# Performance work log

Hardware: AMD Instinct MI355X
Metric: run time of the kernel (lower is better)

## Reference

```python
import jax, jax.numpy as jnp
import numpy as np

BS, P, D, C, ND, K, NC, H = 32, 196, 512, 100, 51, 50, 800, 8
LAMBDA, BETA, EPS = 0.5, 5.5, 1e-5


def _ln(x, g, b):
    m = x.mean(-1, keepdims=True)
    v = jnp.mean((x - m) ** 2, axis=-1, keepdims=True)
    return (x - m) / jnp.sqrt(v + EPS) * g + b


def _norm(x):
    return x / jnp.linalg.norm(x, axis=-1, keepdims=True)


def _bonder(x, kv, Wq, Wk, Wv, Wo, ln1_g, ln1_b, ln2_g, ln2_b, W1, b1, W2, b2):
    # cross-attn block: queries = text prompts [B,N,d], kv = retrieved patch feats [B,M,d]
    B, N, d = x.shape
    M = kv.shape[1]
    dh = d // H
    q = (_ln(x, ln1_g, ln1_b) @ Wq).reshape(B, N, H, dh)
    k = (kv @ Wk).reshape(B, M, H, dh)
    v = (kv @ Wv).reshape(B, M, H, dh)
    att = jax.nn.softmax(jnp.einsum('bnhd,bmhd->bhnm', q, k) / np.sqrt(dh).astype(np.float32), axis=-1)
    o = jnp.einsum('bhnm,bmhd->bnhd', att, v).reshape(B, N, d) @ Wo
    x = x + o
    h = _ln(x, ln2_g, ln2_b)
    return x + jax.nn.gelu(h @ W1 + b1) @ W2 + b2


def _dense_logits(gfeat, local, all_text, mean_text, topk):
    # gfeat [b,d], local [b,p,d], all_text [C,n,d], mean_text [C,d]
    base = gfeat @ mean_text.T                                   # [b,C]
    w = jnp.einsum('bd,bpd->bp', gfeat, local)                   # [b,p]
    atf = jnp.transpose(all_text, (1, 0, 2))                     # [n,C,d]
    v = jax.nn.softmax(jnp.einsum('cd,ncd->nc', mean_text, atf), axis=0)  # [n,C]
    sim = jnp.einsum('bpd,ncd->bcpn', local, atf)                # [b,C,p,n]
    vals, idx = jax.lax.top_k(jnp.transpose(sim, (0, 1, 3, 2)), topk)     # over patch dim
    sim_topk = jnp.transpose(vals, (0, 1, 3, 2))                 # [b,C,k,n]
    idx = jnp.transpose(idx, (0, 1, 3, 2))                       # [b,C,k,n]
    idx_w = idx[:, 0, :, 0]                                      # [b,k]
    w_topk = jax.nn.softmax(jnp.take_along_axis(w, idx_w, axis=1), axis=-1)  # [b,k]
    weight = jnp.einsum('bk,nc->bckn', w_topk, v)                # [b,C,k,n]
    return base + jnp.sum(sim_topk * weight, axis=(-2, -1))


def setup_inputs() -> dict:
    key = jax.random.key(0)
    ks = jax.random.split(key, 12)
    s = 0.02
    labels = jax.random.randint(ks[10], (BS,), 0, C)
    cache_labels = jax.random.randint(ks[11], (NC,), 0, C)
    return {
        'local_feat': jax.random.normal(ks[0], (BS, P, D)),
        'Wa': jnp.eye(D) + s * jax.random.normal(ks[1], (D, D)),
        'text_cache': jax.random.normal(ks[2], (C, ND, D)),
        'Wq': s * jax.random.normal(ks[3], (D, D)),
        'Wk': s * jax.random.normal(ks[4], (D, D)),
        'Wv': s * jax.random.normal(ks[5], (D, D)),
        'Wo': s * jax.random.normal(ks[6], (D, D)),
        'ln1_g': jnp.ones((D,)), 'ln1_b': jnp.zeros((D,)),
        'ln2_g': jnp.ones((D,)), 'ln2_b': jnp.zeros((D,)),
        'W1': s * jax.random.normal(ks[7], (D, 4 * D)), 'b1': jnp.zeros((4 * D,)),
        'W2': s * jax.random.normal(ks[8], (4 * D, D)), 'b2': jnp.zeros((D,)),
        'logit_scale': jnp.asarray(np.log(1.0 / 0.07), jnp.float32),
        'ensemble_scale': jnp.asarray(-2.0, jnp.float32),
        'raw_cache_local_feats': jax.random.normal(ks[9], (NC, P, D)),
        'cache_values': jax.nn.one_hot(cache_labels, C, dtype=jnp.float32),
        'labels': labels,
        'cache_labels': cache_labels,
    }


def reference(local_feat, Wa, text_cache, Wq, Wk, Wv, Wo, ln1_g, ln1_b, ln2_g, ln2_b,
              W1, b1, W2, b2, logit_scale, ensemble_scale, raw_cache_local_feats,
              cache_values, labels, cache_labels):
    bs = local_feat.shape[0]
    adapted_local = _norm(local_feat @ Wa.T)                      # [b,p,d]
    adapted_global = _norm(adapted_local.mean(axis=1))            # [b,d]
    base_text_mean = _norm(jax.lax.stop_gradient(text_cache).mean(axis=1))  # [C,d]
    sim_to_text = jax.lax.stop_gradient(adapted_local @ base_text_mean.T)   # [b,p,C]
    sim_target = sim_to_text[jnp.arange(bs), :, labels]           # [b,p]
    topk_idx = jax.lax.top_k(sim_target, K)[1]
    botk_idx = jax.lax.top_k(-sim_target, K)[1]
    topk_feats = jnp.take_along_axis(adapted_local, topk_idx[:, :, None], axis=1)  # [b,K,d]
    botk_feats = jnp.take_along_axis(adapted_local, botk_idx[:, :, None], axis=1)
    # training branch: bonder on ground-truth class prompts, scatter into bias_full
    l2p = text_cache[labels]                                      # [b,ND,d]
    text_bias = _bonder(l2p, jax.lax.stop_gradient(topk_feats),
                        Wq, Wk, Wv, Wo, ln1_g, ln1_b, ln2_g, ln2_b, W1, b1, W2, b2)
    bias_full = jnp.zeros((bs, C, ND, D), local_feat.dtype).at[jnp.arange(bs), labels].set(text_bias)
    bias_avg = bias_full.mean(axis=0)                             # [C,ND,d]
    refined = text_cache + LAMBDA * bias_avg
    refined_norm = _norm(refined)
    refined_mean_norm = _norm(refined_norm.mean(axis=1))
    ls = jnp.exp(logit_scale)
    inter = ls * _dense_logits(adapted_global, adapted_local, refined_norm, refined_mean_norm, K)
    # tip-adapter cache branch
    cache_adapted = _norm(raw_cache_local_feats @ Wa.T)           # [Nc,p,d]
    cache_sim = jax.lax.stop_gradient(cache_adapted @ base_text_mean.T)
    cache_sim_target = cache_sim[jnp.arange(cache_sim.shape[0]), :, cache_labels]
    cache_topk_idx = jax.lax.top_k(cache_sim_target, K)[1]
    cache_topk_feats = jnp.take_along_axis(cache_adapted, cache_topk_idx[:, :, None], axis=1)
    cache_keys = _norm(cache_topk_feats.mean(axis=1))             # [Nc,d]
    query_keys = _norm(topk_feats.mean(axis=1))                   # [b,d]
    affinity = jnp.exp(-BETA * (1.0 - query_keys @ cache_keys.T))
    intra = affinity @ cache_values                               # [b,C]
    scale = jax.nn.sigmoid(ensemble_scale)
    logits = inter * (1 - scale) + intra * ls * scale
    return (logits, inter, intra, adapted_global, topk_feats, botk_feats, refined_norm)
```

## Files before the change

### kernel.cpp

```cpp
#include <hip/hip_runtime.h>
#include <math.h>

#define DEV static __device__ __forceinline__

typedef __attribute__((ext_vector_type(8))) short short8v;
typedef __attribute__((ext_vector_type(8))) _Float16 half8v;
typedef __attribute__((ext_vector_type(4))) float f32x4;

DEV unsigned encf(float f){ unsigned b=__float_as_uint(f); return b ^ (0x80000000u | (unsigned)((int)b>>31)); }
DEV unsigned long long pkvi(float v, int idx){
  return ((unsigned long long)encf(v)<<32) | (unsigned long long)(0xffffffffu - (unsigned)idx);
}
DEV unsigned long long wave_max_ull(unsigned long long u){
  #pragma unroll
  for (int m=1;m<64;m<<=1){ unsigned long long o = __shfl_xor(u, m); if (o>u) u=o; }
  return u;
}
DEV float wave_sum(float v){
  #pragma unroll
  for (int m=32;m;m>>=1) v += __shfl_xor(v, m);
  return v;
}
DEV float blk_sum256(float v, float* scr){
  v = wave_sum(v);
// ... 76 lines not shown
      for (int i=0;i<8;++i)
        #pragma unroll
        for (int j=0;j<8;++j) acc[i][j] = fmaf(a[i], bb[j], acc[i][j]);
    }
    __syncthreads();
  }

  #pragma unroll
  for (int i=0;i<8;++i){
    int gr = row0 + ((i<4)? (ty*4+i) : (64+ty*4+i-4));
    if (gr >= M) continue;
    #pragma unroll
    for (int jb=0;jb<2;++jb){
      int gc = col0 + (jb? (64+tx*4) : (tx*4));
      float4 vv;
      vv.x = acc[i][jb*4+0]; vv.y = acc[i][jb*4+1]; vv.z = acc[i][jb*4+2]; vv.w = acc[i][jb*4+3];
      if (EPI & 1){
        const float4 bv = *(const float4*)(bias + gc);
        vv.x += bv.x; vv.y += bv.y; vv.z += bv.z; vv.w += bv.w;
      }
      if (EPI & 2){
        vv.x = gelu_f(vv.x); vv.y = gelu_f(vv.y); vv.z = gelu_f(vv.z); vv.w = gelu_f(vv.w);
      }
      if (EPI & 4){
        const float4 rv = *(const float4*)(resid + (size_t)gr*N + gc);
        vv.x += rv.x; vv.y += rv.y; vv.z += rv.z; vv.w += rv.w;
      }
      *(float4*)(Cp + (size_t)gr*N + gc) = vv;
    }
  }
}

template<bool TRANS, bool SUBI>
__global__ __launch_bounds__(256) void k_convw(const float* __restrict__ W,
    unsigned short* __restrict__ hi, unsigned short* __restrict__ lo, int R, int C){
  int n = blockIdx.x;
  int K = TRANS ? R : C;
  for (int k = threadIdx.x; k < K; k += 256){
    float x = TRANS ? W[(size_t)k*C + n] : W[(size_t)n*C + k];
    if (SUBI && k==n) x -= 1.f;
    unsigned short h = f2bf(x);
    hi[(size_t)n*K + k] = h;
    if (lo) lo[(size_t)n*K + k] = f2bf(x - bf2f(h));
  }
}

__global__ __launch_bounds__(256) void k_convw4(
  const float* __restrict__ Wq, const float* __restrict__ Wk,
  const float* __restrict__ Wv, const float* __restrict__ Wo,
  unsigned short* __restrict__ qh, unsigned short* __restrict__ ql,
  unsigned short* __restrict__ kh, unsigned short* __restrict__ kl,
  unsigned short* __restrict__ vh, unsigned short* __restrict__ vl,
  unsigned short* __restrict__ oh, unsigned short* __restrict__ ol)
{
  int n = blockIdx.x;
  const float* W; unsigned short *hi, *lo;
  switch(blockIdx.y){
    case 0: W=Wq; hi=qh; lo=ql; break;
    case 1: W=Wk; hi=kh; lo=kl; break;
    case 2: W=Wv; hi=vh; lo=vl; break;
    default: W=Wo; hi=oh; lo=ol; break;
  }
  for (int k = threadIdx.x; k < 512; k += 256){
    float x = W[(size_t)k*512 + n];
    unsigned short h = f2bf(x);
    hi[(size_t)n*512 + k] = h;
    lo[(size_t)n*512 + k] = f2bf(x - bf2f(h));
  }
}

__global__ __launch_bounds__(256) void k_convd2(const float* __restrict__ Wa, unsigned short* __restrict__ Dfrag){
  int e = blockIdx.x;
  int tile = e>>4, lr = e&15;
  for (int d = threadIdx.x; d < 512; d += 256){
    float x = Wa[(size_t)e*512 + d] - (e==d ? 1.f : 0.f);
    union { _Float16 hh; unsigned short u; } cv;
    cv.hh = (_Float16)x;
    int ks = d>>5, q = (d>>3)&3, el = d&7;
    Dfrag[(size_t)(((tile*16+ks)*64 + q*16 + lr)*8 + el)] = cv.u;
  }
}

template<int EPI>
__global__ __launch_bounds__(256,2) void gemmMF(
  const float* __restrict__ A, const unsigned short* __restrict__ Bhi,
  const unsigned short* __restrict__ Blo, float* __restrict__ Cp,
  const int M, const int N, const int K,
  const float* __restrict__ bias, const float* __restrict__ resid)
{
  __shared__ __align__(16) char sm[32768];
  const int t = threadIdx.x, lane = t&63, wid = t>>6;
  const int row0 = blockIdx.x*128, col0 = blockIdx.y*128;
  f32x4 acc[2][8];
  #pragma unroll
  for (int i=0;i<2;++i)
    #pragma unroll
    for (int j=0;j<8;++j) acc[i][j] = (f32x4){0.f,0.f,0.f,0.f};

  int offA[2], offB[8];
  #pragma unroll
  for (int mt=0; mt<2; ++mt){
    int row = (2*wid+mt)*16 + (lane&15);
    int sp = (lane>>4) ^ ((row>>1)&3);
    offA[mt] = row*64 + sp*16;
  }
  #pragma unroll
  for (int nt=0; nt<8; ++nt){
    int row = nt*16 + (lane&15);
    int sp = (lane>>4) ^ ((row>>1)&3);
    offB[nt] = row*64 + sp*16;
  }

  const int nks = K >> 5;
  for (int ks=0; ks<nks; ++ks){
    #pragma unroll
    for (int i=0;i<2;++i){
      int s = i*256 + t, row = s>>2, sl2 = s&3, phys = sl2 ^ ((row>>1)&3);
      int gr = row0 + row;
      float4 p0 = make_float4(0.f,0.f,0.f,0.f), p1 = p0;
      if (gr < M){
        const float* gp = A + (size_t)gr*K + ks*32 + sl2*8;
        p0 = *(const float4*)gp; p1 = *(const float4*)(gp+4);
      }
      float xs[8] = {p0.x,p0.y,p0.z,p0.w,p1.x,p1.y,p1.z,p1.w};
      union { unsigned short u[8]; float4 f; } uh, ul;
      #pragma unroll
      for (int u=0;u<8;++u){
        unsigned short h = f2bf(xs[u]);
        uh.u[u] = h;
        ul.u[u] = f2bf(xs[u] - bf2f(h));
      }
      *(float4*)(sm + row*64 + phys*16) = uh.f;
      *(float4*)(sm + 8192 + row*64 + phys*16) = ul.f;
    }
    #pragma unroll
    for (int i=0;i<2;++i){
      int s = i*256 + t, row = s>>2, sl2 = s&3, slog = sl2 ^ ((row>>1)&3);
      size_t goff = (size_t)(col0+row)*K + ks*32 + slog*8;
      gld16(Bhi + goff, sm + 16384 + (i*256 + wid*64)*16);
      gld16(Blo + goff, sm + 24576 + (i*256 + wid*64)*16);
    }
    __syncthreads();
    short8v ah0 = *(short8v*)(sm + offA[0]);
    short8v ah1 = *(short8v*)(sm + offA[1]);
    short8v al0 = *(short8v*)(sm + 8192 + offA[0]);
    short8v al1 = *(short8v*)(sm + 8192 + offA[1]);
    #pragma unroll
    for (int nt=0; nt<8; ++nt){
      short8v bh = *(short8v*)(sm + 16384 + offB[nt]);
      short8v bl = *(short8v*)(sm + 24576 + offB[nt]);
      acc[0][nt] = __builtin_amdgcn_mfma_f32_16x16x32_bf16(ah0, bh, acc[0][nt], 0,0,0);
      acc[0][nt] = __builtin_amdgcn_mfma_f32_16x16x32_bf16(ah0, bl, acc[0][nt], 0,0,0);
      acc[0][nt] = __builtin_amdgcn_mfma_f32_16x16x32_bf16(al0, bh, acc[0][nt], 0,0,0);
      acc[1][nt] = __builtin_amdgcn_mfma_f32_16x16x32_bf16(ah1, bh, acc[1][nt], 0,0,0);
      acc[1][nt] = __builtin_amdgcn_mfma_f32_16x16x32_bf16(ah1, bl, acc[1][nt], 0,0,0);
      acc[1][nt] = __builtin_amdgcn_mfma_f32_16x16x32_bf16(al1, bh, acc[1][nt], 0,0,0);
    }
    __syncthreads();
  }

  #pragma unroll
  for (int mt=0; mt<2; ++mt){
    #pragma unroll
    for (int nt=0; nt<8; ++nt){
      int n = col0 + nt*16 + (lane&15);
      int mb = row0 + (2*wid+mt)*16 + (lane>>4)*4;
      #pragma unroll
      for (int j=0;j<4;++j){
        int m = mb + j;
        if (m < M){
          float v = acc[mt][nt][j];
          if (EPI & 1) v += bias[n];
          if (EPI & 2) v = gelu_f(v);
          if (EPI & 4) v += resid[(size_t)m*N + n];
          Cp[(size_t)m*N + n] = v;
        }
      }
    }
  }
}

__global__ __launch_bounds__(256,2) void gemmQKV(
  const float* __restrict__ ln1x, const float* __restrict__ otk,
  const unsigned short* __restrict__ qh, const unsigned short* __restrict__ ql,
  const unsigned short* __restrict__ kh, const unsigned short* __restrict__ kl,
  const unsigned short* __restrict__ vh, const unsigned short* __restrict__ vl,
  float* __restrict__ qb, float* __restrict__ kb, float* __restrict__ vbuf)
{
  __shared__ __align__(16) char sm[32768];
  const int z = blockIdx.z;
  const float* A = (z==0)? ln1x : otk;
  const unsigned short* Bhi = (z==0)? qh : (z==1? kh : vh);
  const unsigned short* Blo = (z==0)? ql : (z==1? kl : vl);
  float* Cp = (z==0)? qb : (z==1? kb : vbuf);
  const int M = (z==0)? 1632 : 1600;
  const int N = 512, K = 512;
  const int t = threadIdx.x, lane = t&63, wid = t>>6;
  const int row0 = blockIdx.x*128, col0 = blockIdx.y*128;
  f32x4 acc[2][8];
  #pragma unroll
  for (int i=0;i<2;++i)
    #pragma unroll
    for (int j=0;j<8;++j) acc[i][j] = (f32x4){0.f,0.f,0.f,0.f};

  int offA[2], offB[8];
  #pragma unroll
  for (int mt=0; mt<2; ++mt){
    int row = (2*wid+mt)*16 + (lane&15);
    int sp = (lane>>4) ^ ((row>>1)&3);
    offA[mt] = row*64 + sp*16;
  }
  #pragma unroll
  for (int nt=0; nt<8; ++nt){
    int row = nt*16 + (lane&15);
    int sp = (lane>>4) ^ ((row>>1)&3);
    offB[nt] = row*64 + sp*16;
  }

  for (int ks=0; ks<16; ++ks){
    #pragma unroll
    for (int i=0;i<2;++i){
      int s = i*256 + t, row = s>>2, sl2 = s&3, phys = sl2 ^ ((row>>1)&3);
      int gr = row0 + row;
      float4 p0 = make_float4(0.f,0.f,0.f,0.f), p1 = p0;
      if (gr < M){
        const float* gp = A + (size_t)gr*K + ks*32 + sl2*8;
        p0 = *(const float4*)gp; p1 = *(const float4*)(gp+4);
      }
      float xs[8] = {p0.x,p0.y,p0.z,p0.w,p1.x,p1.y,p1.z,p1.w};
      union { unsigned short u[8]; float4 f; } uh, ul;
      #pragma unroll
      for (int u=0;u<8;++u){
        unsigned short h = f2bf(xs[u]);
        uh.u[u] = h;
        ul.u[u] = f2bf(xs[u] - bf2f(h));
      }
      *(float4*)(sm + row*64 + phys*16) = uh.f;
      *(float4*)(sm + 8192 + row*64 + phys*16) = ul.f;
    }
    #pragma unroll
    for (int i=0;i<2;++i){
      int s = i*256 + t, row = s>>2, sl2 = s&3, slog = sl2 ^ ((row>>1)&3);
      size_t goff = (size_t)(col0+row)*K + ks*32 + slog*8;
      gld16(Bhi + goff, sm + 16384 + (i*256 + wid*64)*16);
      gld16(Blo + goff, sm + 24576 + (i*256 + wid*64)*16);
    }
    __syncthreads();
    short8v ah0 = *(short8v*)(sm + offA[0]);
    short8v ah1 = *(short8v*)(sm + offA[1]);
    short8v al0 = *(short8v*)(sm + 8192 + offA[0]);
    short8v al1 = *(short8v*)(sm + 8192 + offA[1]);
    #pragma unroll
    for (int nt=0; nt<8; ++nt){
      short8v bh = *(short8v*)(sm + 16384 + offB[nt]);
      short8v bl = *(short8v*)(sm + 24576 + offB[nt]);
      acc[0][nt] = __builtin_amdgcn_mfma_f32_16x16x32_bf16(ah0, bh, acc[0][nt], 0,0,0);
      acc[0][nt] = __builtin_amdgcn_mfma_f32_16x16x32_bf16(ah0, bl, acc[0][nt], 0,0,0);
      acc[0][nt] = __builtin_amdgcn_mfma_f32_16x16x32_bf16(al0, bh, acc[0][nt], 0,0,0);
      acc[1][nt] = __builtin_amdgcn_mfma_f32_16x16x32_bf16(ah1, bh, acc[1][nt], 0,0,0);
      acc[1][nt] = __builtin_amdgcn_mfma_f32_16x16x32_bf16(ah1, bl, acc[1][nt], 0,0,0);
      acc[1][nt] = __builtin_amdgcn_mfma_f32_16x16x32_bf16(al1, bh, acc[1][nt], 0,0,0);
    }
    __syncthreads();
  }

  #pragma unroll
  for (int mt=0; mt<2; ++mt){
    #pragma unroll
    for (int nt=0; nt<8; ++nt){
      int n = col0 + nt*16 + (lane&15);
      int mb = row0 + (2*wid+mt)*16 + (lane>>4)*4;
      #pragma unroll
      for (int j=0;j<4;++j){
        int m = mb + j;
        if (m < M) Cp[(size_t)m*N + n] = acc[mt][nt][j];
      }
    }
  }
}

__global__ __launch_bounds__(512,1) void k_un7(
  const float* __restrict__ raw, const unsigned short* __restrict__ Dfrag,
  const float* __restrict__ zm, const int* __restrict__ clab,
  float* __restrict__ cdot, float* __restrict__ norm2)
{
  __shared__ __align__(16) char Alds[131072];
  __shared__ float n2sq[128];
  __shared__ float n2x[4][128];
  const int t = threadIdx.x, lane = t&63;
  const int wid = t>>6, wm = wid>>2, wn = wid&3;
  const int m0 = blockIdx.x*128;

  {
    const int row = t>>2, sl = t&3;
    const int slg = sl ^ ((row>>1)&3);
    const float* rp = raw + ((size_t)(m0+row))*512 + slg*8;
    const float* zp = zm + (size_t)clab[(m0+row)/196]*512 + slg*8;
    float sq=0.f, cd=0.f;
    for (int ks=0; ks<16; ++ks){
      float4 p0 = *(const float4*)(rp + ks*32);
      float4 p1 = *(const float4*)(rp + ks*32 + 4);
      float4 z0 = *(const float4*)(zp + ks*32);
      float4 z1 = *(const float4*)(zp + ks*32 + 4);
      float xs[8] = {p0.x,p0.y,p0.z,p0.w,p1.x,p1.y,p1.z,p1.w};
      float zs[8] = {z0.x,z0.y,z0.z,z0.w,z1.x,z1.y,z1.z,z1.w};
      union { _Float16 h[8]; f32x4 f; } uh;
      #pragma unroll
      for (int u=0;u<8;++u){
        uh.h[u] = (_Float16)xs[u];
        sq = fmaf(xs[u],xs[u],sq);
        cd = fmaf(xs[u],zs[u],cd);
      }
      *(f32x4*)(Alds + ks*8192 + t*16) = uh.f;
    }
    sq += __shfl_xor(sq,1); sq += __shfl_xor(sq,2);
    cd += __shfl_xor(cd,1); cd += __shfl_xor(cd,2);
    if (sl==0){ n2sq[row] = sq; cdot[m0+row] = cd; }
  }
  __syncthreads();

  int offA[4];
  #pragma unroll
  for (int mt=0; mt<4; ++mt){
    int row = wm*64 + mt*16 + (lane&15);
    int sp = (lane>>4) ^ ((row>>1)&3);
    offA[mt] = row*64 + sp*16;
  }
  const half8v* Dv = (const half8v*)Dfrag;
// ... 86 lines not shown
  for (int r=0;r<nper;++r){ s0 += bp[(size_t)r*512+t]; s1 += bp[(size_t)r*512+t+256]; }
  float ss = blk_sum256(s0*s0+s1*s1, scr);
  float inv = 1.f/sqrtf(ss);
  float v0 = s0*inv, v1 = s1*inv;
  o1[(size_t)g*512+t]=v0; o1[(size_t)g*512+t+256]=v1;
  if (o2){ o2[(size_t)g*512+t]=v0; o2[(size_t)g*512+t+256]=v1; }
}

__global__ __launch_bounds__(256) void k_zmat(const float* __restrict__ btm, const float* __restrict__ Wa, float* __restrict__ z){
  int c = blockIdx.x, t = threadIdx.x;
  float a0=0.f, a1=0.f;
  for (int d=0; d<512; ++d){
    float bv = btm[c*512+d];
    a0 = fmaf(bv, Wa[(size_t)d*512+t], a0);
    a1 = fmaf(bv, Wa[(size_t)d*512+t+256], a1);
  }
  z[c*512+t]=a0; z[c*512+t+256]=a1;
}

__global__ __launch_bounds__(256) void k_dot_bp(const float* __restrict__ AL, const float* __restrict__ vecs,
                                                const int* __restrict__ sel, float* __restrict__ outv, int mode){
  int wid = blockIdx.x*4 + (threadIdx.x>>6);
  int lane = threadIdx.x & 63;
  int b = wid/196;
  int vrow = sel ? sel[b] : (mode ? 0 : b);
  const float* a = AL + (size_t)wid*512 + lane*8;
  const float* v = vecs + (size_t)vrow*512 + lane*8;
  float4 a0 = *(const float4*)a, a1 = *(const float4*)(a+4);
  float4 v0 = *(const float4*)v, v1 = *(const float4*)(v+4);
  float s = a0.x*v0.x + a0.y*v0.y + a0.z*v0.z + a0.w*v0.w
          + a1.x*v1.x + a1.y*v1.y + a1.z*v1.z + a1.w*v1.w;
  s = wave_sum(s);
  if (lane==0) outv[wid] = s;
}

__global__ __launch_bounds__(256) void k_dot2(const float* __restrict__ AL, const float* __restrict__ AGw,
                                              const float* __restrict__ RN00,
                                              float* __restrict__ wbp, float* __restrict__ sLw){
  int wid = blockIdx.x*4 + (threadIdx.x>>6);
  int lane = threadIdx.x & 63;
  int b = wid/196;
  const float* a = AL + (size_t)wid*512 + lane*8;
  const float* v = AGw + (size_t)b*512 + lane*8;
  const float* w = RN00 + lane*8;
  float4 a0=*(const float4*)a, a1=*(const float4*)(a+4);
  float4 v0=*(const float4*)v, v1=*(const float4*)(v+4);
  float4 w0=*(const float4*)w, w1=*(const float4*)(w+4);
  float s1 = a0.x*v0.x+a0.y*v0.y+a0.z*v0.z+a0.w*v0.w + a1.x*v1.x+a1.y*v1.y+a1.z*v1.z+a1.w*v1.w;
  float s2 = a0.x*w0.x+a0.y*w0.y+a0.z*w0.z+a0.w*w0.w + a1.x*w1.x+a1.y*w1.y+a1.z*w1.z+a1.w*w1.w;
  s1 = wave_sum(s1); s2 = wave_sum(s2);
  if (lane==0){ wbp[wid] = s1; sLw[wid] = s2; }
}

__global__ __launch_bounds__(64) void k_topbot(const float* __restrict__ st, int* __restrict__ tki, int* __restrict__ bki){
  int b = blockIdx.x, lane = threadIdx.x;
  float v[4];
  #pragma unroll
  for (int s2=0;s2<4;++s2){ int p = lane + 64*s2; v[s2] = (p<196)? st[b*196+p] : -INFINITY; }
  for (int k=0;k<50;++k){
    unsigned long long best = pkvi(v[0], lane);
    { unsigned long long cc=pkvi(v[1],lane+64);  if(cc>best)best=cc; }
    { unsigned long long cc=pkvi(v[2],lane+128); if(cc>best)best=cc; }
    { unsigned long long cc=pkvi(v[3],lane+192); if(cc>best)best=cc; }
    best = wave_max_ull(best);
    int widx = (int)(0xffffffffu - (unsigned)(best & 0xffffffffu));
    if (lane==0) tki[b*50+k] = widx;
    if ((widx & 63)==lane) v[widx>>6] = -INFINITY;
  }
  #pragma unroll
  for (int s2=0;s2<4;++s2){ int p = lane + 64*s2; v[s2] = (p<196)? -st[b*196+p] : -INFINITY; }
  for (int k=0;k<50;++k){
    unsigned long long best = pkvi(v[0], lane);
    { unsigned long long cc=pkvi(v[1],lane+64);  if(cc>best)best=cc; }
    { unsigned long long cc=pkvi(v[2],lane+128); if(cc>best)best=cc; }
    { unsigned long long cc=pkvi(v[3],lane+192); if(cc>best)best=cc; }
    best = wave_max_ull(best);
    int widx = (int)(0xffffffffu - (unsigned)(best & 0xffffffffu));
    if (lane==0) bki[b*50+k] = widx;
    if ((widx & 63)==lane) v[widx>>6] = -INFINITY;
  }
}

__global__ __launch_bounds__(256) void k_gather_tb(const float* __restrict__ AL, const int* __restrict__ tki, const int* __restrict__ bki,
                                                   float* __restrict__ otk, float* __restrict__ obk, float* __restrict__ qk){
  __shared__ float scr[4];
  int b = blockIdx.x, t = threadIdx.x;
  float a0=0.f, a1=0.f;
  for (int k=0;k<50;++k){
    int pt = tki[b*50+k];
    const float* rp = AL + ((size_t)b*196+pt)*512;
    float x0 = rp[t], x1 = rp[t+256];
    otk[((size_t)b*50+k)*512 + t] = x0; otk[((size_t)b*50+k)*512 + t+256] = x1;
    a0 += x0; a1 += x1;
    int pb = bki[b*50+k];
    const float* rb = AL + ((size_t)b*196+pb)*512;
    obk[((size_t)b*50+k)*512 + t] = rb[t]; obk[((size_t)b*50+k)*512 + t+256] = rb[t+256];
  }
  float ss = blk_sum256(a0*a0+a1*a1, scr);
  float inv = 1.f/sqrtf(ss);
  qk[b*512+t] = a0*inv; qk[b*512+t+256] = a1*inv;
}

__global__ __launch_bounds__(256) void k_gather_x(const float* __restrict__ tc, const int* __restrict__ labels, float* __restrict__ xb){
  int r = blockIdx.x, t = threadIdx.x;
  int b = r/51, n = r%51;
  int lab = labels[b];
  const float* src = tc + ((size_t)lab*51 + n)*512;
  xb[(size_t)r*512+t] = src[t]; xb[(size_t)r*512+t+256] = src[t+256];
}

__global__ __launch_bounds__(256) void k_layernorm(const float* __restrict__ in, float* __restrict__ out,
                                                   const float* __restrict__ g, const float* __restrict__ be){
  __shared__ float scr[4];
  int r = blockIdx.x, t = threadIdx.x;
  const float* p = in + (size_t)r*512;
  float x0=p[t], x1=p[t+256];
  float s = blk_sum256(x0+x1, scr);
  float mean = s*(1.f/512.f);
  float ss = blk_sum256(x0*x0+x1*x1, scr);
  float var = ss*(1.f/512.f) - mean*mean;
  float inv = 1.f/sqrtf(var + 1e-5f);
  out[(size_t)r*512+t]     = (x0-mean)*inv*g[t]     + be[t];
  out[(size_t)r*512+t+256] = (x1-mean)*inv*g[t+256] + be[t+256];
}

__global__ __launch_bounds__(256) void k_attn(const float* __restrict__ qb, const float* __restrict__ kb,
                                              const float* __restrict__ vb, float* __restrict__ ob){
  int b = blockIdx.x, h = blockIdx.y, t = threadIdx.x;
  __shared__ float qh[51][65];
  __shared__ float kh[50][65];
  __shared__ float vh[50][65];
  __shared__ float S[51][52];
  for (int f=t; f<51*64; f+=256){ int n=f>>6, d=f&63; qh[n][d] = qb[((size_t)(b*51+n))*512 + h*64 + d]; }
  for (int f=t; f<50*64; f+=256){ int m=f>>6, d=f&63;
    kh[m][d] = kb[((size_t)(b*50+m))*512 + h*64 + d];
    vh[m][d] = vb[((size_t)(b*50+m))*512 + h*64 + d];
  }
  __syncthreads();
  for (int f=t; f<51*50; f+=256){
    int n=f/50, m=f%50;
    float s=0.f;
    #pragma unroll 8
    for (int d=0; d<64; ++d) s = fmaf(qh[n][d], kh[m][d], s);
    S[n][m] = s*0.125f;
  }
  __syncthreads();
  int w = t>>6, lane = t&63;
  for (int n=w; n<51; n+=4){
    float x = (lane<50)? S[n][lane] : -INFINITY;
    float mx = x;
    #pragma unroll
    for (int m2=32;m2;m2>>=1) mx = fmaxf(mx, __shfl_xor(mx,m2));
    float e = (lane<50)? expf(x-mx) : 0.f;
    float se = wave_sum(e);
    if (lane<50) S[n][lane] = e/se;
  }
  __syncthreads();
  for (int f=t; f<51*64; f+=256){
    int n=f>>6, d=f&63;
    float s=0.f;
    #pragma unroll 10
    for (int m=0;m<50;++m) s = fmaf(S[n][m], vh[m][d], s);
    ob[((size_t)(b*51+n))*512 + h*64 + d] = s;
  }
}

__global__ __launch_bounds__(256) void k_refined(const float* __restrict__ tc, const float* __restrict__ TB,
                                                 const int* __restrict__ labels, float* __restrict__ RN,
                                                 unsigned short* __restrict__ RNbf){
  __shared__ float scr[4];
  __shared__ int labL[32];
  int blk = blockIdx.x, t = threadIdx.x;
  int c = blk/51, n = blk%51;
  if (t<32) labL[t] = labels[t];
  __syncthreads();
  float r0=0.f, r1=0.f;
  for (int b=0;b<32;++b){
    if (labL[b]==c){
      const float* tb = TB + ((size_t)(b*51+n))*512;
      r0 += tb[t]; r1 += tb[t+256];
    }
  }
  const float* tcp = tc + ((size_t)(c*51+n))*512;
  r0 = tcp[t]     + r0*(1.f/64.f);
  r1 = tcp[t+256] + r1*(1.f/64.f);
  float ss = blk_sum256(r0*r0+r1*r1, scr);
  float inv = 1.f/sqrtf(ss);
  float v0 = r0*inv, v1 = r1*inv;
  RN[((size_t)(c*51+n))*512+t]     = v0;
  RN[((size_t)(c*51+n))*512+t+256] = v1;
  size_t br = (size_t)c*64 + n;
  RNbf[br*512 + t]     = f2bf(v0);
  RNbf[br*512 + t+256] = f2bf(v1);
}

__global__ __launch_bounds__(256) void k_vsm(const float* __restrict__ RN, const float* __restrict__ RMN, float* __restrict__ vsm){
  __shared__ float sv[51];
  int c = blockIdx.x, t = threadIdx.x, w = t>>6, lane = t&63;
  for (int n=w; n<51; n+=4){
    const float* a = RN + ((size_t)(c*51+n))*512 + lane*8;
    const float* m = RMN + (size_t)c*512 + lane*8;
    float4 a0=*(const float4*)a, a1=*(const float4*)(a+4);
    float4 m0=*(const float4*)m, m1=*(const float4*)(m+4);
    float s = a0.x*m0.x+a0.y*m0.y+a0.z*m0.z+a0.w*m0.w + a1.x*m1.x+a1.y*m1.y+a1.z*m1.z+a1.w*m1.w;
    s = wave_sum(s);
    if (lane==0) sv[n]=s;
  }
  __syncthreads();
  if (t<64){
    float x = (t<51)? sv[t] : -INFINITY;
    float mx = x;
    #pragma unroll
    for (int m2=32;m2;m2>>=1) mx = fmaxf(mx, __shfl_xor(mx,m2));
    float e = (t<51)? expf(x-mx) : 0.f;
    float se = wave_sum(e);
    if (t<51) vsm[c*51+t] = e/se;
  }
}

__global__ __launch_bounds__(64) void k_wtopk(const float* __restrict__ sLg,
                                              const float* __restrict__ wbp, float* __restrict__ wtk){
  __shared__ int idxL[50];
  int b = blockIdx.x, lane = threadIdx.x;
  float v[4];
  #pragma unroll
  for (int s2=0;s2<4;++s2){ int p = lane+64*s2; v[s2] = (p<196)? sLg[b*196+p] : -INFINITY; }
  for (int k=0;k<50;++k){
    unsigned long long best = pkvi(v[0], lane);
    { unsigned long long cc=pkvi(v[1],lane+64);  if(cc>best)best=cc; }
    { unsigned long long cc=pkvi(v[2],lane+128); if(cc>best)best=cc; }
    { unsigned long long cc=pkvi(v[3],lane+192); if(cc>best)best=cc; }
    best = wave_max_ull(best);
    int widx = (int)(0xffffffffu - (unsigned)(best & 0xffffffffu));
    if (lane==0) idxL[k]=widx;
    if ((widx&63)==lane) v[widx>>6] = -INFINITY;
  }
  __syncthreads();
  float wv = (lane<50)? wbp[b*196 + idxL[lane]] : -INFINITY;
  float mx = wv;
  #pragma unroll
  for (int m2=32;m2;m2>>=1) mx = fmaxf(mx, __shfl_xor(mx,m2));
  float e = (lane<50)? expf(wv-mx) : 0.f;
  float se = wave_sum(e);
  if (lane<50) wtk[b*50+lane] = e/se;
}

// ... 89 lines not shown
        *(f32x4*)(smem + addr) = acc[mt][nt];
      }
    }
  }
  __syncthreads();

  const int n = wid*16 + (lane>>2);
  const int q = lane&3;
  float v[64];
  if (n < 51){
    #pragma unroll
    for (int i=0;i<16;++i){
      int p = q*64 + i*4;
      int addr = ((n<<10) + (p<<2)) ^ ((((n&7)^q)&7)<<4);
      *(f32x4*)&v[i*4] = *(f32x4*)(smem + addr);
    }
  } else {
    #pragma unroll
    for (int i=0;i<64;++i) v[i] = -INFINITY;
  }
  if (q==3){
    #pragma unroll
    for (int j=4;j<64;++j) v[j] = -INFINITY;
  }

  #pragma unroll
  for (int k=2;k<=64;k<<=1){
    #pragma unroll
    for (int j=k>>1;j>=1;j>>=1){
      #pragma unroll
      for (int i=0;i<64;++i){
        if ((i&j)==0){
          int p2 = i|j;
          float a=v[i], bb=v[p2];
          if ((i&k)!=0){ v[i]=fminf(a,bb); v[p2]=fmaxf(a,bb); }
          else         { v[i]=fmaxf(a,bb); v[p2]=fminf(a,bb); }
        }
      }
    }
  }
  #pragma unroll
  for (int i=0;i<32;++i){
    float pa = dppf<0xB1>(v[63-i]);
    float pb = dppf<0xB1>(v[i]);
    v[i]    = fmaxf(v[i], pa);
    v[63-i] = fmaxf(v[63-i], pb);
  }
  #pragma unroll
  for (int j=32;j>=1;j>>=1){
    #pragma unroll
    for (int i=0;i<64;++i){
      if ((i&j)==0){ int p2=i|j; float a=v[i],bb=v[p2]; v[i]=fmaxf(a,bb); v[p2]=fminf(a,bb); }
    }
  }
  #pragma unroll
  for (int i=0;i<32;++i){
    float pa = dppf<0x4E>(v[63-i]);
    float pb = dppf<0x4E>(v[i]);
    v[i]    = fmaxf(v[i], pa);
    v[63-i] = fmaxf(v[63-i], pb);
  }
  #pragma unroll
  for (int j=32;j>=1;j>>=1){
    #pragma unroll
    for (int i=0;i<64;++i){
      if ((i&j)==0){ int p2=i|j; float a=v[i],bb=v[p2]; v[i]=fmaxf(a,bb); v[p2]=fminf(a,bb); }
    }
  }

  float s = 0.f;
  #pragma unroll
  for (int r=0;r<50;++r) s = fmaf(wtkS[r], v[r], s);
  float val = (q==0 && n<51) ? vsm[c*51+n]*s : 0.f;
  val = wave_sum(val);
  if (lane==0) red[wid] = val;
  __syncthreads();
  if (t==0){
    float ls = expf(lsp[0]);
    interw[b*100+c] = ls*(red[4] + red[0]+red[1]+red[2]+red[3]);
  }
}

__global__ __launch_bounds__(256) void k_cache_sel(const float* __restrict__ cdot, const float* __restrict__ norm2,
                                                   const float* __restrict__ raw, float* __restrict__ rbar){
  __shared__ int idxL[50];
  __shared__ float invL[50];
  int i = blockIdx.x, t = threadIdx.x;
  if (t < 64){
    int lane = t;
    float v[4];
    #pragma unroll
    for (int s2=0;s2<4;++s2){
      int p = lane+64*s2;
      v[s2] = (p<196)? cdot[(size_t)i*196+p] * (1.f/sqrtf(norm2[(size_t)i*196+p])) : -INFINITY;
    }
    for (int k=0;k<50;++k){
      unsigned long long best = pkvi(v[0], lane);
      { unsigned long long cc=pkvi(v[1],lane+64);  if(cc>best)best=cc; }
      { unsigned long long cc=pkvi(v[2],lane+128); if(cc>best)best=cc; }
      { unsigned long long cc=pkvi(v[3],lane+192); if(cc>best)best=cc; }
      best = wave_max_ull(best);
      int widx = (int)(0xffffffffu - (unsigned)(best & 0xffffffffu));
      if (lane==0){ idxL[k]=widx; invL[k] = 1.f/sqrtf(norm2[(size_t)i*196+widx]); }
      if ((widx&63)==lane) v[widx>>6] = -INFINITY;
    }
  }
  __syncthreads();
  float a0=0.f, a1=0.f;
  for (int k=0;k<50;++k){
    int p = idxL[k]; float iv = invL[k];
    const float* rp = raw + ((size_t)i*196+p)*512;
    a0 = fmaf(rp[t], iv, a0);
    a1 = fmaf(rp[t+256], iv, a1);
  }
  rbar[(size_t)i*512+t]=a0; rbar[(size_t)i*512+t+256]=a1;
}

__global__ __launch_bounds__(256) void k_aff(const float* __restrict__ qk, const float* __restrict__ ck, float* __restrict__ aff){
  int gid = blockIdx.x*4 + (threadIdx.x>>6);
  int lane = threadIdx.x&63;
  int b = gid/800, i = gid%800;
  const float* a = qk + (size_t)b*512 + lane*8;
  const float* v = ck + (size_t)i*512 + lane*8;
  float4 a0=*(const float4*)a, a1=*(const float4*)(a+4);
  float4 v0=*(const float4*)v, v1=*(const float4*)(v+4);
  float s = a0.x*v0.x+a0.y*v0.y+a0.z*v0.z+a0.w*v0.w + a1.x*v1.x+a1.y*v1.y+a1.z*v1.z+a1.w*v1.w;
  s = wave_sum(s);
  if (lane==0) aff[gid] = expf(-5.5f*(1.f - s));
}

__global__ __launch_bounds__(128) void k_intra(const float* __restrict__ aff, const float* __restrict__ cv, float* __restrict__ intra){
  __shared__ float affL[800];
  int b = blockIdx.x, t = threadIdx.x;
  for (int f=t; f<800; f+=128) affL[f] = aff[b*800+f];
  __syncthreads();
  if (t<100){
    float s=0.f;
    for (int i=0;i<800;++i) s = fmaf(affL[i], cv[(size_t)i*100+t], s);
    intra[b*100+t]=s;
  }
}

__global__ void k_final(const float* __restrict__ interw, const float* __restrict__ intraw,
                        const float* __restrict__ lsp, const float* __restrict__ esp, float* __restrict__ outp){
  int idx = blockIdx.x*256 + threadIdx.x;
  if (idx < 3200){
    float ls = expf(lsp[0]);
    float sc = 1.f/(1.f + expf(-esp[0]));
    float iv = interw[idx], ia = intraw[idx];
    outp[idx]        = iv*(1.f-sc) + ia*ls*sc;
    outp[3200+idx]   = iv;
    outp[6400+idx]   = ia;
  }
}

extern "C" void kernel_launch(void* const* d_in, const int* in_sizes, int n_in,
                              void* d_out, int out_size, void* d_ws, size_t ws_size,
                              hipStream_t stream)
{
  (void)in_sizes; (void)n_in; (void)out_size; (void)ws_size;
  const float* lf   = (const float*)d_in[0];
  const float* Wa   = (const float*)d_in[1];
  const float* tc   = (const float*)d_in[2];
  const float* Wq   = (const float*)d_in[3];
  const float* Wk   = (const float*)d_in[4];
  const float* Wv   = (const float*)d_in[5];
  const float* Wo   = (const float*)d_in[6];
  const float* ln1g = (const float*)d_in[7];
  const float* ln1b = (const float*)d_in[8];
  const float* ln2g = (const float*)d_in[9];
  const float* ln2b = (const float*)d_in[10];
  const float* W1   = (const float*)d_in[11];
  const float* b1   = (const float*)d_in[12];
  const float* W2   = (const float*)d_in[13];
  const float* b2   = (const float*)d_in[14];
  const float* lsp  = (const float*)d_in[15];
  const float* esp  = (const float*)d_in[16];
  const float* raw  = (const float*)d_in[17];
  const float* cv   = (const float*)d_in[18];
  const int* labels = (const int*)d_in[19];
  const int* clab   = (const int*)d_in[20];

  float* out = (float*)d_out;
  float* outAG = out + 9600;
  float* outTK = out + 25984;
  float* outBK = out + 845184;
  float* outRN = out + 1664384;

  float* wsf = (float*)d_ws;
  size_t o = 0;
  #define WALLOC(name, n) float* name = wsf + o; o += (size_t)(n);
  WALLOC(AL,    6272*512)
  WALLOC(xb,    1632*512)
  WALLOC(ln1x,  1632*512)
  WALLOC(qb,    1632*512)
  WALLOC(kb,    1600*512)
  WALLOC(vbuf,  1600*512)
  WALLOC(ob,    1632*512)
  WALLOC(x2,    1632*512)
  WALLOC(h2,    1632*512)
  WALLOC(y1g,   (size_t)1632*2048)
  WALLOC(TB,    1632*512)
  WALLOC(btm,   100*512)
  WALLOC(zm,    100*512)
  WALLOC(RMN,   100*512)
  WALLOC(vsm,   5100)
  WALLOC(st,    6272)
  WALLOC(wbp,   6272)
  WALLOC(sLw,   6272)
  WALLOC(AGw,   32*512)
  WALLOC(qkb,   32*512)
  WALLOC(wtk,   1600)
  WALLOC(norm2, 156800)
  WALLOC(cdot,  156800)
  WALLOC(rbar,  800*512)
  WALLOC(mbuf,  800*512)
  WALLOC(ckb,   800*512)
  WALLOC(aff,   25600)
  WALLOC(interw,3200)
  WALLOC(intraw,3200)
  #undef WALLOC
  int* tki = (int*)(wsf + o); o += 1600;
  int* bki = (int*)(wsf + o); o += 1600;
  unsigned short* ALbf = (unsigned short*)(wsf + o); o += (size_t)32*256*512/2;
  unsigned short* RNbf = (unsigned short*)(wsf + o); o += (size_t)100*64*512/2;
  #define WALLOC16(name, n) unsigned short* name = (unsigned short*)(wsf + o); o += ((size_t)(n))/2;
  WALLOC16(waHi, 262144)  WALLOC16(waLo, 262144)
  WALLOC16(wqHi, 262144)  WALLOC16(wqLo, 262144)
  WALLOC16(wkHi, 262144)  WALLOC16(wkLo, 262144)
  WALLOC16(wvHi, 262144)  WALLOC16(wvLo, 262144)
  WALLOC16(woHi, 262144)  WALLOC16(woLo, 262144)
  WALLOC16(w1Hi, 1048576) WALLOC16(w1Lo, 1048576)
  WALLOC16(w2Hi, 1048576) WALLOC16(w2Lo, 1048576)
  WALLOC16(dfrag, 262144)
  #undef WALLOC16

  k_convw<false,false><<<dim3(512), dim3(256), 0, stream>>>(Wa, waHi, waLo, 512,512);
  k_convw4<<<dim3(512,4), dim3(256), 0, stream>>>(Wq,Wk,Wv,Wo, wqHi,wqLo, wkHi,wkLo, wvHi,wvLo, woHi,woLo);
  k_convw<true ,false><<<dim3(2048), dim3(256), 0, stream>>>(W1, w1Hi, w1Lo, 512,2048);
  k_convw<true ,false><<<dim3(512), dim3(256), 0, stream>>>(W2, w2Hi, w2Lo, 2048,512);
  k_convd2<<<dim3(512), dim3(256), 0, stream>>>(Wa, dfrag);

  hipMemsetAsync(ALbf, 0, (size_t)32*256*512*2, stream);
  hipMemsetAsync(RNbf, 0, (size_t)100*64*512*2, stream);

  gemm128<true,0><<<dim3(49,4), dim3(256), 0, stream>>>(lf, Wa, AL, 6272,512,512, nullptr,nullptr);
  k_rownorm<<<dim3(6272), dim3(256), 0, stream>>>(AL, AL, ALbf, 6272);
  k_meanrows_norm<<<dim3(32), dim3(256), 0, stream>>>(AL, 196, AGw, outAG);
  k_meanrows_norm<<<dim3(100), dim3(256), 0, stream>>>(tc, 51, btm, (float*)nullptr);
  k_zmat<<<dim3(100), dim3(256), 0, stream>>>(btm, Wa, zm);
  k_dot_bp<<<dim3(1568), dim3(256), 0, stream>>>(AL, btm, labels, st, 0);
  k_topbot<<<dim3(32), dim3(64), 0, stream>>>(st, tki, bki);
  k_gather_tb<<<dim3(32), dim3(256), 0, stream>>>(AL, tki, bki, outTK, outBK, qkb);
  k_gather_x<<<dim3(1632), dim3(256), 0, stream>>>(tc, labels, xb);
  k_layernorm<<<dim3(1632), dim3(256), 0, stream>>>(xb, ln1x, ln1g, ln1b);
  gemmQKV<<<dim3(13,4,3), dim3(256), 0, stream>>>(ln1x, outTK, wqHi,wqLo, wkHi,wkLo, wvHi,wvLo, qb, kb, vbuf);
  k_attn<<<dim3(32,8), dim3(256), 0, stream>>>(qb, kb, vbuf, ob);
  gemmMF<4><<<dim3(13,4), dim3(256), 0, stream>>>(ob, woHi, woLo, x2, 1632,512,512, nullptr, xb);
  k_layernorm<<<dim3(1632), dim3(256), 0, stream>>>(x2, h2, ln2g, ln2b);
  gemmMF<3><<<dim3(13,16), dim3(256), 0, stream>>>(h2, w1Hi, w1Lo, y1g, 1632,2048,512, b1, nullptr);
  gemmMF<5><<<dim3(13,4), dim3(256), 0, stream>>>(y1g, w2Hi, w2Lo, TB, 1632,512,2048, b2, x2);
  k_refined<<<dim3(5100), dim3(256), 0, stream>>>(tc, TB, labels, outRN, RNbf);
  k_meanrows_norm<<<dim3(100), dim3(256), 0, stream>>>(outRN, 51, RMN, (float*)nullptr);
  k_vsm<<<dim3(100), dim3(256), 0, stream>>>(outRN, RMN, vsm);
  k_dot2<<<dim3(1568), dim3(256), 0, stream>>>(AL, AGw, outRN, wbp, sLw);
  k_wtopk<<<dim3(32), dim3(64), 0, stream>>>(sLw, wbp, wtk);
  k_dense3<<<dim3(100,32), dim3(256), 0, stream>>>(ALbf, RNbf, RMN, AGw, vsm, wtk, lsp, interw);
  k_un7<<<dim3(1225), dim3(512), 0, stream>>>(raw, dfrag, zm, clab, cdot, norm2);
  k_cache_sel<<<dim3(800), dim3(256), 0, stream>>>(cdot, norm2, raw, rbar);
  gemmMF<0><<<dim3(7,4), dim3(256), 0, stream>>>(rbar, waHi, waLo, mbuf, 800,512,512, nullptr,nullptr);
  k_rownorm<<<dim3(800), dim3(256), 0, stream>>>(mbuf, ckb, (unsigned short*)nullptr, 800);
  k_aff<<<dim3(6400), dim3(256), 0, stream>>>(qkb, ckb, aff);
  k_intra<<<dim3(32), dim3(128), 0, stream>>>(aff, cv, intraw);
  k_final<<<dim3(13), dim3(256), 0, stream>>>(interw, intraw, lsp, esp, out);
}
```

Measured before the change: 1.105 ms.

## Emit bf16 hi/lo activation splits in producers and load GEMM A tiles directly

```diff
diff --git a/kernel.cpp b/kernel.cpp
--- a/kernel.cpp
+++ b/kernel.cpp
@@ -182,9 +182,10 @@
 }
 
 template<int EPI>
-__global__ __launch_bounds__(256,2) void gemmMF(
-  const float* __restrict__ A, const unsigned short* __restrict__ Bhi,
-  const unsigned short* __restrict__ Blo, float* __restrict__ Cp,
+__global__ __launch_bounds__(256,2) void gemmAB(
+  const unsigned short* __restrict__ Ahi, const unsigned short* __restrict__ Alo,
+  const unsigned short* __restrict__ Bhi, const unsigned short* __restrict__ Blo,
+  float* __restrict__ Cp, unsigned short* __restrict__ Chi, unsigned short* __restrict__ Clo,
   const int M, const int N, const int K,
   const float* __restrict__ bias, const float* __restrict__ resid)
 {
@@ -215,30 +216,14 @@
   for (int ks=0; ks<nks; ++ks){
     #pragma unroll
     for (int i=0;i<2;++i){
-      int s = i*256 + t, row = s>>2, sl2 = s&3, phys = sl2 ^ ((row>>1)&3);
-      int gr = row0 + row;
-      float4 p0 = make_float4(0.f,0.f,0.f,0.f), p1 = p0;
-      if (gr < M){
-        const float* gp = A + (size_t)gr*K + ks*32 + sl2*8;
-        p0 = *(const float4*)gp; p1 = *(const float4*)(gp+4);
-      }
-      float xs[8] = {p0.x,p0.y,p0.z,p0.w,p1.x,p1.y,p1.z,p1.w};
-      union { unsigned short u[8]; float4 f; } uh, ul;
-      #pragma unroll
-      for (int u=0;u<8;++u){
-        unsigned short h = f2bf(xs[u]);
-        uh.u[u] = h;
-        ul.u[u] = f2bf(xs[u] - bf2f(h));
-      }
-      *(float4*)(sm + row*64 + phys*16) = uh.f;
-      *(float4*)(sm + 8192 + row*64 + phys*16) = ul.f;
-    }
-    #pragma unroll
-    for (int i=0;i<2;++i){
       int s = i*256 + t, row = s>>2, sl2 = s&3, slog = sl2 ^ ((row>>1)&3);
-      size_t goff = (size_t)(col0+row)*K + ks*32 + slog*8;
-      gld16(Bhi + goff, sm + 16384 + (i*256 + wid*64)*16);
-      gld16(Blo + goff, sm + 24576 + (i*256 + wid*64)*16);
+      size_t ga = (size_t)(row0+row)*K + ks*32 + slog*8;
+      size_t gb = (size_t)(col0+row)*K + ks*32 + slog*8;
+      int dst = (i*256 + wid*64)*16;
+      gld16(Ahi + ga, sm + dst);
+      gld16(Alo + ga, sm + 8192 + dst);
+      gld16(Bhi + gb, sm + 16384 + dst);
+      gld16(Blo + gb, sm + 24576 + dst);
     }
     __syncthreads();
     short8v ah0 = *(short8v*)(sm + offA[0]);
@@ -273,15 +258,22 @@
           if (EPI & 1) v += bias[n];
           if (EPI & 2) v = gelu_f(v);
           if (EPI & 4) v += resid[(size_t)m*N + n];
-          Cp[(size_t)m*N + n] = v;
+          if (EPI & 8){
+            unsigned short h = f2bf(v);
+            Chi[(size_t)m*N + n] = h;
+            Clo[(size_t)m*N + n] = f2bf(v - bf2f(h));
+          } else {
+            Cp[(size_t)m*N + n] = v;
+          }
         }
       }
     }
   }
 }
 
-__global__ __launch_bounds__(256,2) void gemmQKV(
-  const float* __restrict__ ln1x, const float* __restrict__ otk,
+__global__ __launch_bounds__(256,2) void gemmABQKV(
+  const unsigned short* __restrict__ lnH, const unsigned short* __restrict__ lnL,
+  const unsigned short* __restrict__ tkH, const unsigned short* __restrict__ tkL,
   const unsigned short* __restrict__ qh, const unsigned short* __restrict__ ql,
   const unsigned short* __restrict__ kh, const unsigned short* __restrict__ kl,
   const unsigned short* __restrict__ vh, const unsigned short* __restrict__ vl,
@@ -289,12 +281,13 @@
 {
   __shared__ __align__(16) char sm[32768];
   const int z = blockIdx.z;
-  const float* A = (z==0)? ln1x : otk;
+  const unsigned short* Ahi = (z==0)? lnH : tkH;
+  const unsigned short* Alo = (z==0)? lnL : tkL;
   const unsigned short* Bhi = (z==0)? qh : (z==1? kh : vh);
   const unsigned short* Blo = (z==0)? ql : (z==1? kl : vl);
   float* Cp = (z==0)? qb : (z==1? kb : vbuf);
   const int M = (z==0)? 1632 : 1600;
-  const int N = 512, K = 512;
+  const int K = 512, N = 512;
   const int t = threadIdx.x, lane = t&63, wid = t>>6;
   const int row0 = blockIdx.x*128, col0 = blockIdx.y*128;
   f32x4 acc[2][8];
@@ -320,30 +313,14 @@
   for (int ks=0; ks<16; ++ks){
     #pragma unroll
     for (int i=0;i<2;++i){
-      int s = i*256 + t, row = s>>2, sl2 = s&3, phys = sl2 ^ ((row>>1)&3);
-      int gr = row0 + row;
-      float4 p0 = make_float4(0.f,0.f,0.f,0.f), p1 = p0;
-      if (gr < M){
-        const float* gp = A + (size_t)gr*K + ks*32 + sl2*8;
-        p0 = *(const float4*)gp; p1 = *(const float4*)(gp+4);
-      }
-      float xs[8] = {p0.x,p0.y,p0.z,p0.w,p1.x,p1.y,p1.z,p1.w};
-      union { unsigned short u[8]; float4 f; } uh, ul;
-      #pragma unroll
-      for (int u=0;u<8;++u){
-        unsigned short h = f2bf(xs[u]);
-        uh.u[u] = h;
-        ul.u[u] = f2bf(xs[u] - bf2f(h));
-      }
-      *(float4*)(sm + row*64 + phys*16) = uh.f;
-      *(float4*)(sm + 8192 + row*64 + phys*16) = ul.f;
-    }
-    #pragma unroll
-    for (int i=0;i<2;++i){
       int s = i*256 + t, row = s>>2, sl2 = s&3, slog = sl2 ^ ((row>>1)&3);
-      size_t goff = (size_t)(col0+row)*K + ks*32 + slog*8;
-      gld16(Bhi + goff, sm + 16384 + (i*256 + wid*64)*16);
-      gld16(Blo + goff, sm + 24576 + (i*256 + wid*64)*16);
+      size_t ga = (size_t)(row0+row)*K + ks*32 + slog*8;
+      size_t gb = (size_t)(col0+row)*K + ks*32 + slog*8;
+      int dst = (i*256 + wid*64)*16;
+      gld16(Ahi + ga, sm + dst);
+      gld16(Alo + ga, sm + 8192 + dst);
+      gld16(Bhi + gb, sm + 16384 + dst);
+      gld16(Blo + gb, sm + 24576 + dst);
     }
     __syncthreads();
     short8v ah0 = *(short8v*)(sm + offA[0]);
@@ -596,7 +573,8 @@
 }
 
 __global__ __launch_bounds__(256) void k_gather_tb(const float* __restrict__ AL, const int* __restrict__ tki, const int* __restrict__ bki,
-                                                   float* __restrict__ otk, float* __restrict__ obk, float* __restrict__ qk){
+                                                   float* __restrict__ otk, float* __restrict__ obk, float* __restrict__ qk,
+                                                   unsigned short* __restrict__ tkH, unsigned short* __restrict__ tkL){
   __shared__ float scr[4];
   int b = blockIdx.x, t = threadIdx.x;
   float a0=0.f, a1=0.f;
@@ -604,11 +582,15 @@
     int pt = tki[b*50+k];
     const float* rp = AL + ((size_t)b*196+pt)*512;
     float x0 = rp[t], x1 = rp[t+256];
-    otk[((size_t)b*50+k)*512 + t] = x0; otk[((size_t)b*50+k)*512 + t+256] = x1;
+    size_t ro = ((size_t)b*50+k)*512;
+    otk[ro + t] = x0; otk[ro + t+256] = x1;
+    unsigned short h0 = f2bf(x0), h1 = f2bf(x1);
+    tkH[ro + t] = h0;      tkL[ro + t]     = f2bf(x0 - bf2f(h0));
+    tkH[ro + t+256] = h1;  tkL[ro + t+256] = f2bf(x1 - bf2f(h1));
     a0 += x0; a1 += x1;
     int pb = bki[b*50+k];
     const float* rb = AL + ((size_t)b*196+pb)*512;
-    obk[((size_t)b*50+k)*512 + t] = rb[t]; obk[((size_t)b*50+k)*512 + t+256] = rb[t+256];
+    obk[ro + t] = rb[t]; obk[ro + t+256] = rb[t+256];
   }
   float ss = blk_sum256(a0*a0+a1*a1, scr);
   float inv = 1.f/sqrtf(ss);
@@ -623,8 +605,9 @@
   xb[(size_t)r*512+t] = src[t]; xb[(size_t)r*512+t+256] = src[t+256];
 }
 
-__global__ __launch_bounds__(256) void k_layernorm(const float* __restrict__ in, float* __restrict__ out,
-                                                   const float* __restrict__ g, const float* __restrict__ be){
+__global__ __launch_bounds__(256) void k_layernorm2(const float* __restrict__ in,
+                                                    unsigned short* __restrict__ hi, unsigned short* __restrict__ lo,
+                                                    const float* __restrict__ g, const float* __restrict__ be){
   __shared__ float scr[4];
   int r = blockIdx.x, t = threadIdx.x;
   const float* p = in + (size_t)r*512;
@@ -634,12 +617,16 @@
   float ss = blk_sum256(x0*x0+x1*x1, scr);
   float var = ss*(1.f/512.f) - mean*mean;
   float inv = 1.f/sqrtf(var + 1e-5f);
-  out[(size_t)r*512+t]     = (x0-mean)*inv*g[t]     + be[t];
-  out[(size_t)r*512+t+256] = (x1-mean)*inv*g[t+256] + be[t+256];
-}
-
-__global__ __launch_bounds__(256) void k_attn(const float* __restrict__ qb, const float* __restrict__ kb,
-                                              const float* __restrict__ vb, float* __restrict__ ob){
+  float v0 = (x0-mean)*inv*g[t]     + be[t];
+  float v1 = (x1-mean)*inv*g[t+256] + be[t+256];
+  unsigned short h0 = f2bf(v0), h1 = f2bf(v1);
+  hi[(size_t)r*512+t]     = h0;  lo[(size_t)r*512+t]     = f2bf(v0 - bf2f(h0));
+  hi[(size_t)r*512+t+256] = h1;  lo[(size_t)r*512+t+256] = f2bf(v1 - bf2f(h1));
+}
+
+__global__ __launch_bounds__(256) void k_attn2(const float* __restrict__ qb, const float* __restrict__ kb,
+                                               const float* __restrict__ vb,
+                                               unsigned short* __restrict__ obH, unsigned short* __restrict__ obL){
   int b = blockIdx.x, h = blockIdx.y, t = threadIdx.x;
   __shared__ float qh[51][65];
   __shared__ float kh[50][65];
@@ -675,7 +662,9 @@
     float s=0.f;
     #pragma unroll 10
     for (int m=0;m<50;++m) s = fmaf(S[n][m], vh[m][d], s);
-    ob[((size_t)(b*51+n))*512 + h*64 + d] = s;
+    size_t idx = ((size_t)(b*51+n))*512 + h*64 + d;
+    unsigned short hh = f2bf(s);
+    obH[idx] = hh; obL[idx] = f2bf(s - bf2f(hh));
   }
 }
 
@@ -931,7 +920,8 @@
 }
 
 __global__ __launch_bounds__(256) void k_cache_sel(const float* __restrict__ cdot, const float* __restrict__ norm2,
-                                                   const float* __restrict__ raw, float* __restrict__ rbar){
+                                                   const float* __restrict__ raw,
+                                                   unsigned short* __restrict__ rbH, unsigned short* __restrict__ rbL){
   __shared__ int idxL[50];
   __shared__ float invL[50];
   int i = blockIdx.x, t = threadIdx.x;
@@ -962,7 +952,9 @@
     a0 = fmaf(rp[t], iv, a0);
     a1 = fmaf(rp[t+256], iv, a1);
   }
-  rbar[(size_t)i*512+t]=a0; rbar[(size_t)i*512+t+256]=a1;
+  unsigned short h0 = f2bf(a0), h1 = f2bf(a1);
+  rbH[(size_t)i*512+t]     = h0;  rbL[(size_t)i*512+t]     = f2bf(a0 - bf2f(h0));
+  rbH[(size_t)i*512+t+256] = h1;  rbL[(size_t)i*512+t+256] = f2bf(a1 - bf2f(h1));
 }
 
 __global__ __launch_bounds__(256) void k_aff(const float* __restrict__ qk, const float* __restrict__ ck, float* __restrict__ aff){
@@ -1041,14 +1033,10 @@
   #define WALLOC(name, n) float* name = wsf + o; o += (size_t)(n);
   WALLOC(AL,    6272*512)
   WALLOC(xb,    1632*512)
-  WALLOC(ln1x,  1632*512)
   WALLOC(qb,    1632*512)
   WALLOC(kb,    1600*512)
   WALLOC(vbuf,  1600*512)
-  WALLOC(ob,    1632*512)
   WALLOC(x2,    1632*512)
-  WALLOC(h2,    1632*512)
-  WALLOC(y1g,   (size_t)1632*2048)
   WALLOC(TB,    1632*512)
   WALLOC(btm,   100*512)
   WALLOC(zm,    100*512)
@@ -1062,7 +1050,6 @@
   WALLOC(wtk,   1600)
   WALLOC(norm2, 156800)
   WALLOC(cdot,  156800)
-  WALLOC(rbar,  800*512)
   WALLOC(mbuf,  800*512)
   WALLOC(ckb,   800*512)
   WALLOC(aff,   25600)
@@ -1073,7 +1060,7 @@
   int* bki = (int*)(wsf + o); o += 1600;
   unsigned short* ALbf = (unsigned short*)(wsf + o); o += (size_t)32*256*512/2;
   unsigned short* RNbf = (unsigned short*)(wsf + o); o += (size_t)100*64*512/2;
-  #define WALLOC16(name, n) unsigned short* name = (unsigned short*)(wsf + o); o += ((size_t)(n))/2;
+  #define WALLOC16(name, n) unsigned short* name = (unsigned short*)(wsf + o); o += ((size_t)(n)+1)/2;
   WALLOC16(waHi, 262144)  WALLOC16(waLo, 262144)
   WALLOC16(wqHi, 262144)  WALLOC16(wqLo, 262144)
   WALLOC16(wkHi, 262144)  WALLOC16(wkLo, 262144)
@@ -1082,6 +1069,12 @@
   WALLOC16(w1Hi, 1048576) WALLOC16(w1Lo, 1048576)
   WALLOC16(w2Hi, 1048576) WALLOC16(w2Lo, 1048576)
   WALLOC16(dfrag, 262144)
+  WALLOC16(ln1H, 851968)  WALLOC16(ln1L, 851968)
+  WALLOC16(h2H,  851968)  WALLOC16(h2L,  851968)
+  WALLOC16(obH,  851968)  WALLOC16(obL,  851968)
+  WALLOC16(tkH,  851968)  WALLOC16(tkL,  851968)
+  WALLOC16(y1H,  3407872) WALLOC16(y1L,  3407872)
+  WALLOC16(rbH,  458752)  WALLOC16(rbL,  458752)
   #undef WALLOC16
 
   k_convw<false,false><<<dim3(512), dim3(256), 0, stream>>>(Wa, waHi, waLo, 512,512);
@@ -1090,8 +1083,7 @@
   k_convw<true ,false><<<dim3(512), dim3(256), 0, stream>>>(W2, w2Hi, w2Lo, 2048,512);
   k_convd2<<<dim3(512), dim3(256), 0, stream>>>(Wa, dfrag);
 
-  hipMemsetAsync(ALbf, 0, (size_t)32*256*512*2, stream);
-  hipMemsetAsync(RNbf, 0, (size_t)100*64*512*2, stream);
+  hipMemsetAsync(ALbf, 0, ((size_t)32*256*512 + (size_t)100*64*512)*2, stream);
 
   gemm128<true,0><<<dim3(49,4), dim3(256), 0, stream>>>(lf, Wa, AL, 6272,512,512, nullptr,nullptr);
   k_rownorm<<<dim3(6272), dim3(256), 0, stream>>>(AL, AL, ALbf, 6272);
@@ -1100,15 +1092,15 @@
   k_zmat<<<dim3(100), dim3(256), 0, stream>>>(btm, Wa, zm);
   k_dot_bp<<<dim3(1568), dim3(256), 0, stream>>>(AL, btm, labels, st, 0);
   k_topbot<<<dim3(32), dim3(64), 0, stream>>>(st, tki, bki);
-  k_gather_tb<<<dim3(32), dim3(256), 0, stream>>>(AL, tki, bki, outTK, outBK, qkb);
+  k_gather_tb<<<dim3(32), dim3(256), 0, stream>>>(AL, tki, bki, outTK, outBK, qkb, tkH, tkL);
   k_gather_x<<<dim3(1632), dim3(256), 0, stream>>>(tc, labels, xb);
-  k_layernorm<<<dim3(1632), dim3(256), 0, stream>>>(xb, ln1x, ln1g, ln1b);
-  gemmQKV<<<dim3(13,4,3), dim3(256), 0, stream>>>(ln1x, outTK, wqHi,wqLo, wkHi,wkLo, wvHi,wvLo, qb, kb, vbuf);
-  k_attn<<<dim3(32,8), dim3(256), 0, stream>>>(qb, kb, vbuf, ob);
-  gemmMF<4><<<dim3(13,4), dim3(256), 0, stream>>>(ob, woHi, woLo, x2, 1632,512,512, nullptr, xb);
-  k_layernorm<<<dim3(1632), dim3(256), 0, stream>>>(x2, h2, ln2g, ln2b);
-  gemmMF<3><<<dim3(13,16), dim3(256), 0, stream>>>(h2, w1Hi, w1Lo, y1g, 1632,2048,512, b1, nullptr);
-  gemmMF<5><<<dim3(13,4), dim3(256), 0, stream>>>(y1g, w2Hi, w2Lo, TB, 1632,512,2048, b2, x2);
+  k_layernorm2<<<dim3(1632), dim3(256), 0, stream>>>(xb, ln1H, ln1L, ln1g, ln1b);
+  gemmABQKV<<<dim3(13,4,3), dim3(256), 0, stream>>>(ln1H,ln1L, tkH,tkL, wqHi,wqLo, wkHi,wkLo, wvHi,wvLo, qb, kb, vbuf);
+  k_attn2<<<dim3(32,8), dim3(256), 0, stream>>>(qb, kb, vbuf, obH, obL);
+  gemmAB<4><<<dim3(13,4), dim3(256), 0, stream>>>(obH, obL, woHi, woLo, x2, nullptr, nullptr, 1632,512,512, nullptr, xb);
+  k_layernorm2<<<dim3(1632), dim3(256), 0, stream>>>(x2, h2H, h2L, ln2g, ln2b);
+  gemmAB<11><<<dim3(13,16), dim3(256), 0, stream>>>(h2H, h2L, w1Hi, w1Lo, nullptr, y1H, y1L, 1632,2048,512, b1, nullptr);
+  gemmAB<5><<<dim3(13,4), dim3(256), 0, stream>>>(y1H, y1L, w2Hi, w2Lo, TB, nullptr, nullptr, 1632,512,2048, b2, x2);
   k_refined<<<dim3(5100), dim3(256), 0, stream>>>(tc, TB, labels, outRN, RNbf);
   k_meanrows_norm<<<dim3(100), dim3(256), 0, stream>>>(outRN, 51, RMN, (float*)nullptr);
   k_vsm<<<dim3(100), dim3(256), 0, stream>>>(outRN, RMN, vsm);
@@ -1116,8 +1108,8 @@
   k_wtopk<<<dim3(32), dim3(64), 0, stream>>>(sLw, wbp, wtk);
   k_dense3<<<dim3(100,32), dim3(256), 0, stream>>>(ALbf, RNbf, RMN, AGw, vsm, wtk, lsp, interw);
   k_un7<<<dim3(1225), dim3(512), 0, stream>>>(raw, dfrag, zm, clab, cdot, norm2);
-  k_cache_sel<<<dim3(800), dim3(256), 0, stream>>>(cdot, norm2, raw, rbar);
-  gemmMF<0><<<dim3(7,4), dim3(256), 0, stream>>>(rbar, waHi, waLo, mbuf, 800,512,512, nullptr,nullptr);
+  k_cache_sel<<<dim3(800), dim3(256), 0, stream>>>(cdot, norm2, raw, rbH, rbL);
+  gemmAB<0><<<dim3(7,4), dim3(256), 0, stream>>>(rbH, rbL, waHi, waLo, mbuf, nullptr, nullptr, 800,512,512, nullptr, nullptr);
   k_rownorm<<<dim3(800), dim3(256), 0, stream>>>(mbuf, ckb, (unsigned short*)nullptr, 800);
   k_aff<<<dim3(6400), dim3(256), 0, stream>>>(qkb, ckb, aff);
   k_intra<<<dim3(32), dim3(128), 0, stream>>>(aff, cv, intraw);
```

New measurement: 1.060 ms. -4.0%, faster.
